# Optimization experiments

Measured on AMD Instinct MI355X. Metric: run time of the kernel, lower is better.

## Reference

```python
import jax, jax.numpy as jnp
import numpy as np

DECAY = 0.99
EPS = 1e-05


def setup_inputs() -> dict:
    key = jax.random.key(0)
    k1, k2 = jax.random.split(key)
    B, L, D, K = 8, 2048, 512, 4096
    x = jax.random.normal(k1, (B, L, D), dtype=jnp.float32)
    # variance_scaling(scale=1, fan_in, uniform): U(-limit, limit), limit = sqrt(3/fan_in)
    limit = np.sqrt(3.0 / D)
    codebook = jax.random.uniform(k2, (K, D), dtype=jnp.float32, minval=-limit, maxval=limit)
    return {
        "x": x,
        "codebook": codebook,
        "hidden_cluster": jnp.zeros((K,), jnp.float32),
        "hidden_dw": jnp.zeros((K, D), jnp.float32),
        "count": jnp.zeros((), jnp.float32),
    }


def reference(x, codebook, hidden_cluster, hidden_dw, count):
    K, D = codebook.shape
    B, L, _ = x.shape
    # avoids materializing the (B,L,K,D) broadcast the naive cdist creates)
    x2 = jnp.sum(x * x, axis=-1, keepdims=True)                  # (B,L,1)
    c2 = jnp.sum(codebook * codebook, axis=-1)                   # (K,)
    xc = jnp.einsum("bld,kd->blk", x, codebook)                  # (B,L,K)
    d2 = x2 - 2.0 * xc + c2
    indices = jnp.argmin(d2, axis=-1)                            # (B,L) int
    flat_idx = indices.reshape(-1)

    # cluster_counts = one_hot(indices).sum((0,1)) as a scatter-add
    cluster_counts = jnp.zeros((K,), jnp.float32).at[flat_idx].add(1.0)
    # dw = einsum('bln,bld->nd', one_hot, x) as a scatter-add of x rows
    dw = jnp.zeros((K, D), jnp.float32).at[flat_idx].add(x.reshape(-1, D))

    decay = jnp.asarray(DECAY, x.dtype)
    one = jnp.ones([], x.dtype)
    count_new = count + 1.0
    bias = one - decay ** count_new

    hidden_cluster_new = hidden_cluster * decay + (one - decay) * cluster_counts
    avg_cluster = hidden_cluster_new / bias
    hidden_dw_new = hidden_dw * decay + (one - decay) * dw
    avg_dw = hidden_dw_new / bias

    N = jnp.sum(avg_cluster)
    cc = (avg_cluster + EPS) / (N + K * EPS) * N
    codebook_new = avg_dw / cc[:, None]

    # quantized = one_hot(indices) @ codebook_new == gather
    q = codebook_new[indices]                                    # (B,L,D)
    quantized = x + jax.lax.stop_gradient(q - x)
    # optax.l2_loss(x, quantized).mean() == 0.5*(x-quantized)^2 mean
    codebook_loss = 0.5 * jnp.mean(jnp.square(x - quantized))
    return quantized, codebook_loss, indices
```

## Files before the change

kernel.cpp:

```cpp
#include <hip/hip_runtime.h>
#include <math.h>

#define BL 16384
#define D  512
#define K  4096
#define NCHB 8
#define XLOFF 8388608

#define OFF_C2    0
#define OFF_X2    (16<<10)
#define OFF_CNT   (80<<10)
#define OFF_AVGC  (96<<10)
#define OFF_SCAL  (112<<10)
#define OFF_IDX16 (116<<10)
#define OFF_KEYS  (160<<10)
#define OFF_CAND  (288<<10)
#define OFF_CBP   (576<<10)
#define OFF_CBN_FB (256<<10)

typedef _Float16 f16x8 __attribute__((ext_vector_type(8)));
typedef float    f32x4 __attribute__((ext_vector_type(4)));
#define MFMA16(a,b,c) __builtin_amdgcn_mfma_f32_16x16x32_f16(a,b,c,0,0,0)


__global__ void rowsq_all(const float* __restrict__ x, const float* __restrict__ cb,
                          float* __restrict__ x2, float* __restrict__ c2)
{
    int b    = blockIdx.x;
    int lane = threadIdx.x;
    const float* p; float* o; int row;
    if (b < K) { p = cb; o = c2; row = b; }
    else       { p = x;  o = x2; row = b - K; }
    p += (size_t)row * D;
    float s = 0.f;
#pragma unroll
    for (int j = 0; j < D / 64; ++j) {
        float v = p[lane + j * 64];
        s = fmaf(v, v, s);
    }
#pragma unroll
    for (int off = 32; off > 0; off >>= 1)
        s += __shfl_down(s, off, 64);
    if (lane == 0) o[row] = s;
}

__global__ __launch_bounds__(256) void rescore_kernel(
    const float* __restrict__ x, const float* __restrict__ cb,
    const float* __restrict__ x2, const float* __restrict__ c2,
    const unsigned short* __restrict__ cand,
    unsigned long long* __restrict__ keys,
    float* __restrict__ counts, unsigned short* __restrict__ idx16)
{
    int t = blockIdx.x * 256 + threadIdx.x;
    int row = t >> 3, ci = t & 7;
    int idx = cand[(size_t)row * 8 + ci];
    const float* xp = x  + (size_t)row * D;
    const float* cp = cb + (size_t)idx * D;
    float acc = 0.f;
#pragma unroll 4
    for (int k0 = 0; k0 < D; k0 += 4) {
        float4 xv = *(const float4*)(xp + k0);
        float4 cv = *(const float4*)(cp + k0);
        acc = fmaf(xv.x, cv.x, acc);
        acc = fmaf(xv.y, cv.y, acc);
        acc = fmaf(xv.z, cv.z, acc);
        acc = fmaf(xv.w, cv.w, acc);
    }
    float wv = x2[row] - 2.0f * acc;
    float dd = wv + c2[idx];
    unsigned long long key =
        ((unsigned long long)__float_as_uint(dd) << 12) | (unsigned long long)idx;
#pragma unroll
    for (int m = 1; m < 8; m <<= 1) {
        unsigned long long o = __shfl_xor(key, m, 64);
        key = o < key ? o : key;
    }
    if ((t & 7) == 0) {
        keys[row] = key;
        int kf = (int)(key & 0xFFFULL);
        idx16[row] = (unsigned short)kf;
        atomicAdd(&counts[kf], 1.0f);
    }
}


__device__ __forceinline__ void load_lds16(const unsigned short* g, unsigned short* l) {
    __builtin_amdgcn_global_load_lds(
        (const __attribute__((address_space(1))) unsigned int*)(g),
        (__attribute__((address_space(3))) unsigned int*)(l), 16, 0, 0);
}

__global__ __launch_bounds__(256) void split_interleave(
    const float* __restrict__ x, const float* __restrict__ cb,
    unsigned short* __restrict__ xp, unsigned short* __restrict__ cbp)
{
    int gw   = blockIdx.x * 4 + (threadIdx.x >> 6);
    int lane = threadIdx.x & 63;
    int rl   = lane >> 3;
    int p    = lane & 7;
    const float* src; int nr, c, r0; bool isX;
    if (gw < 16384) { c = gw >> 11; r0 = (gw & 2047) * 8; src = x;  nr = BL; isX = true; }
    else { int lw = gw - 16384; c = lw >> 9; r0 = (lw & 511) * 8; src = cb; nr = K; isX = false; }
    int r = r0 + rl;
    int g = p ^ rl;
    const float* sp = src + (size_t)r * D + c * 64 + g * 8;
    float4 f0 = *(const float4*)sp, f1 = *(const float4*)(sp + 4);
    float f[8] = {f0.x,f0.y,f0.z,f0.w,f1.x,f1.y,f1.z,f1.w};
    __align__(16) _Float16 oh[8], ol[8];
#pragma unroll
    for (int i = 0; i < 8; ++i) {
        _Float16 h = (_Float16)f[i];
        oh[i] = h;
        ol[i] = (_Float16)(f[i] - (float)h);
    }
    size_t off = ((size_t)(c * nr + r) * 8 + p) * 8;
    if (isX) {
        *(uint4*)(xp + off)         = *(const uint4*)oh;
        *(uint4*)(xp + XLOFF + off) = *(const uint4*)ol;
    } else {
        *(uint4*)(cbp + off) = *(const uint4*)oh;
    }
}

__global__ __launch_bounds__(256, 2) void argmin_mfma(
    const unsigned short* __restrict__ xp, const unsigned short* __restrict__ cbp,
    const float* __restrict__ x2, const float* __restrict__ c2,
    unsigned short* __restrict__ cand)
{
    __shared__ __align__(16) unsigned short sAh[128 * 64];
    __shared__ __align__(16) unsigned short sAl[128 * 64];
    __shared__ __align__(16) unsigned short sB [256 * 64];
    __shared__ __align__(16) float c2s[1024];
    __shared__ float x2s[128];

    const int tid = threadIdx.x;
    const int l   = tid & 63;
    const int w   = tid >> 6;
    const int wm  = w >> 1;
    const int wn  = w & 1;
    const int q   = l >> 4;
    const int cc  = l & 15;
    const int row0 = blockIdx.x * 128;
    const int nb   = blockIdx.y * 1024;

    if (tid < 128) x2s[tid] = x2[row0 + tid];
#pragma unroll
    for (int j = 0; j < 4; ++j) c2s[j * 256 + tid] = c2[nb + j * 256 + tid];

    int rdA[4], rdB[8];
#pragma unroll
    for (int t = 0; t < 4; ++t) {
        int ra = wm * 64 + t * 16 + cc;
        rdA[t] = ra * 128 + ((q ^ (ra & 7)) * 16);
    }
#pragma unroll
    for (int t = 0; t < 8; ++t) {
        int rb = wn * 128 + t * 16 + cc;
        rdB[t] = rb * 128 + ((q ^ (rb & 7)) * 16);
    }

    unsigned long long s1a = ~0ULL, s2a = ~0ULL, s1b = ~0ULL, s2b = ~0ULL;
    unsigned long long s1c = ~0ULL, s2c = ~0ULL, s1d = ~0ULL, s2d = ~0ULL;

#pragma unroll 1
    for (int n0 = 0; n0 < 4; ++n0) {
        f32x4 acc[4][8];
#pragma unroll
        for (int tm = 0; tm < 4; ++tm)
#pragma unroll
            for (int tn = 0; tn < 8; ++tn) { f32x4 z = {0.f,0.f,0.f,0.f}; acc[tm][tn] = z; }

#pragma unroll 1
        for (int c = 0; c < NCHB; ++c) {
            __syncthreads();
            {
                size_t abase = ((size_t)c * BL + row0) * 64;
                size_t bbase = ((size_t)(c * K + nb + n0 * 256)) * 64;
#pragma unroll
                for (int i = 0; i < 4; ++i) {
                    load_lds16(xp + abase + i * 2048 + tid * 8, &sAh[i * 2048 + tid * 8]);
                    load_lds16(xp + XLOFF + abase + i * 2048 + tid * 8, &sAl[i * 2048 + tid * 8]);
                }
#pragma unroll
                for (int i = 0; i < 8; ++i)
                    load_lds16(cbp + bbase + i * 2048 + tid * 8, &sB[i * 2048 + tid * 8]);
            }
            __syncthreads();
#pragma unroll
            for (int kh = 0; kh < 2; ++kh) {
                const int xo = kh * 64;
                f16x8 Ah[4], Al[4], Bf[8];
#pragma unroll
                for (int t = 0; t < 4; ++t) {
                    Ah[t] = *(const f16x8*)((const char*)sAh + (rdA[t] ^ xo));
                    Al[t] = *(const f16x8*)((const char*)sAl + (rdA[t] ^ xo));
                }
#pragma unroll
                for (int t = 0; t < 8; ++t)
                    Bf[t] = *(const f16x8*)((const char*)sB + (rdB[t] ^ xo));
#pragma unroll
                for (int tm = 0; tm < 4; ++tm)
#pragma unroll
                    for (int tn = 0; tn < 8; ++tn)
                        acc[tm][tn] = MFMA16(Ah[tm], Bf[tn], acc[tm][tn]);
#pragma unroll
                for (int tm = 0; tm < 4; ++tm)
#pragma unroll
                    for (int tn = 0; tn < 8; ++tn)
                        acc[tm][tn] = MFMA16(Al[tm], Bf[tn], acc[tm][tn]);
            }
        }

        {
            unsigned long long k1[16], k2[16];
#pragma unroll
            for (int s = 0; s < 16; ++s) { k1[s] = ~0ULL; k2[s] = ~0ULL; }
            float c2v[8];
#pragma unroll
            for (int tn = 0; tn < 8; ++tn)
                c2v[tn] = c2s[n0 * 256 + wn * 128 + tn * 16 + cc];
#pragma unroll
            for (int tm = 0; tm < 4; ++tm)
#pragma unroll
                for (int r = 0; r < 4; ++r) {
                    const int s = tm * 4 + r;
                    float x2v = x2s[wm * 64 + tm * 16 + q * 4 + r];
#pragma unroll
                    for (int tn = 0; tn < 8; ++tn) {
                        unsigned col = nb + n0 * 256 + wn * 128 + tn * 16 + cc;
                        float dd = (x2v - 2.0f * acc[tm][tn][r]) + c2v[tn];
                        unsigned long long key =
                            ((unsigned long long)__float_as_uint(dd) << 12) | col;
                        if (key < k1[s]) { k2[s] = k1[s]; k1[s] = key; }
                        else if (key < k2[s]) { k2[s] = key; }
                    }
                }

#pragma unroll
            for (int s = 0; s < 16; ++s) {
#pragma unroll
                for (int m = 1; m < 16; m <<= 1) {
                    unsigned long long o1 = __shfl_xor(k1[s], m, 64);
                    unsigned long long o2 = __shfl_xor(k2[s], m, 64);
                    unsigned long long lf = k1[s] > o1 ? k1[s] : o1;
                    unsigned long long ws_ = k2[s] < o2 ? k2[s] : o2;
                    k1[s] = k1[s] < o1 ? k1[s] : o1;
                    k2[s] = lf < ws_ ? lf : ws_;
                }
            }
            unsigned long long m1 = k1[0], m2 = k2[0];
#pragma unroll
            for (int s = 1; s < 16; ++s) {
                if (cc == s) { m1 = k1[s]; m2 = k2[s]; }
            }
            if (n0 == 0)      { s1a = m1; s2a = m2; }
            else if (n0 == 1) { s1b = m1; s2b = m2; }
            else if (n0 == 2) { s1c = m1; s2c = m2; }
            else              { s1d = m1; s2d = m2; }
        }
    }

    __syncthreads();
    unsigned long long* sc = (unsigned long long*)sAh;
    {
        int rloc = (cc >> 2) * 16 + q * 4 + (cc & 3);
        int r    = wm * 64 + rloc;
        size_t base = (size_t)((r * 2 + wn) * 4) * 2;
        sc[base + 0] = s1a; sc[base + 1] = s2a;
        sc[base + 2] = s1b; sc[base + 3] = s2b;
        sc[base + 4] = s1c; sc[base + 5] = s2c;
        sc[base + 6] = s1d; sc[base + 7] = s2d;
    }
    __syncthreads();
    if (tid < 128) {
        unsigned long long m1 = ~0ULL, m2 = ~0ULL;
#pragma unroll
        for (int j = 0; j < 8; ++j) {
            unsigned long long b1 = sc[(size_t)(tid * 8 + j) * 2 + 0];
            unsigned long long b2 = sc[(size_t)(tid * 8 + j) * 2 + 1];
            unsigned long long lf  = m1 > b1 ? m1 : b1;
            unsigned long long ws_ = m2 < b2 ? m2 : b2;
            m1 = m1 < b1 ? m1 : b1;
            m2 = lf < ws_ ? lf : ws_;
        }
        size_t base = (size_t)(row0 + tid) * 8 + blockIdx.y * 2;
        cand[base + 0] = (unsigned short)(m1 & 0xFFFULL);
        cand[base + 1] = (unsigned short)(m2 & 0xFFFULL);
    }
}

__global__ __launch_bounds__(256) void argmin_fb(
    const float* __restrict__ x, const float* __restrict__ cb,
    const float* __restrict__ x2, const float* __restrict__ c2,
    unsigned long long* __restrict__ keys)
{
    __shared__ __align__(16) float As[32][68];
    __shared__ __align__(16) float Bs[32][68];
    __shared__ float rv[64][16];
    __shared__ int   ri[64][16];

    const int tid  = threadIdx.x;
    const int tx   = tid & 15;
    const int ty   = tid >> 4;
    const int row0 = blockIdx.x * 64;
    const int nb   = blockIdx.y * 1024;

    float x2r[4];
#pragma unroll
    for (int m = 0; m < 4; ++m) x2r[m] = x2[row0 + ty * 4 + m];

    float minv[4]; int mini[4];
#pragma unroll
    for (int m = 0; m < 4; ++m) { minv[m] = 3.4028235e38f; mini[m] = 0; }

    for (int n0 = 0; n0 < 1024; n0 += 64) {
        float acc[4][4];
#pragma unroll
        for (int m = 0; m < 4; ++m)
#pragma unroll
            for (int n = 0; n < 4; ++n) acc[m][n] = 0.f;

        for (int d0 = 0; d0 < D; d0 += 32) {
            __syncthreads();
#pragma unroll
            for (int j = 0; j < 2; ++j) {
                int v   = j * 256 + tid;
                int row = v >> 3;
                int col = (v & 7) * 4;
                float4 av = *(const float4*)(x  + (size_t)(row0 + row) * D + d0 + col);
                As[col + 0][row] = av.x; As[col + 1][row] = av.y;
                As[col + 2][row] = av.z; As[col + 3][row] = av.w;
                float4 bv = *(const float4*)(cb + (size_t)(nb + n0 + row) * D + d0 + col);
                Bs[col + 0][row] = bv.x; Bs[col + 1][row] = bv.y;
                Bs[col + 2][row] = bv.z; Bs[col + 3][row] = bv.w;
            }
            __syncthreads();
#pragma unroll
            for (int kk = 0; kk < 32; ++kk) {
                float4 a4 = *(const float4*)&As[kk][ty * 4];
                float4 b4 = *(const float4*)&Bs[kk][tx * 4];
                float a_[4] = { a4.x, a4.y, a4.z, a4.w };
                float b_[4] = { b4.x, b4.y, b4.z, b4.w };
#pragma unroll
                for (int m = 0; m < 4; ++m)
#pragma unroll
                    for (int n = 0; n < 4; ++n)
                        acc[m][n] = fmaf(a_[m], b_[n], acc[m][n]);
            }
        }
#pragma unroll
        for (int n = 0; n < 4; ++n) {
            int kidx = nb + n0 + tx * 4 + n;
            float c2k = c2[kidx];
#pragma unroll
            for (int m = 0; m < 4; ++m) {
                float wv = x2r[m] - 2.0f * acc[m][n];
                float dd = wv + c2k;
                if (dd < minv[m]) { minv[m] = dd; mini[m] = kidx; }
            }
        }
    }
#pragma unroll
    for (int m = 0; m < 4; ++m) { rv[ty * 4 + m][tx] = minv[m]; ri[ty * 4 + m][tx] = mini[m]; }
    __syncthreads();
    if (tid < 64) {
        float bv = rv[tid][0]; int bi = ri[tid][0];
#pragma unroll
        for (int j = 1; j < 16; ++j) {
            float v = rv[tid][j]; int ii = ri[tid][j];
            if (v < bv || (v == bv && ii < bi)) { bv = v; bi = ii; }
        }
        unsigned long long key =
            ((unsigned long long)__float_as_uint(bv) << 12) | (unsigned long long)bi;
        atomicMin(&keys[row0 + tid], key);
    }
}


__global__ void count_kernel(const unsigned long long* __restrict__ keys,
                             float* __restrict__ counts, unsigned short* __restrict__ idx16)
{
    int i = blockIdx.x * 256 + threadIdx.x;
    int k = (int)(keys[i] & 0xFFFULL);
    idx16[i] = (unsigned short)k;
    atomicAdd(&counts[k], 1.0f);
}

__global__ __launch_bounds__(256) void ema_cluster_kernel(
    const float* __restrict__ hc, const float* __restrict__ counts,
    const float* __restrict__ countp, float* __restrict__ avgc, float* __restrict__ Nout)
{
    __shared__ float sm[256];
    int i = blockIdx.x * 256 + threadIdx.x;
    const float om = 1.0f - 0.99f;
    float bias = 1.0f - powf(0.99f, countp[0] + 1.0f);
    float a = (hc[i] * 0.99f + om * counts[i]) / bias;
    avgc[i] = a;
    sm[threadIdx.x] = a;
    __syncthreads();
    for (int s = 128; s > 0; s >>= 1) {
        if (threadIdx.x < s) sm[threadIdx.x] += sm[threadIdx.x + s];
        __syncthreads();
    }
    if (threadIdx.x == 0) atomicAdd(Nout, sm[0]);
}

__global__ __launch_bounds__(256) void code_update_kernel(
    const float* __restrict__ x, const unsigned short* __restrict__ idx16,
    const float* __restrict__ hdw, const float* __restrict__ avgc,
    const float* __restrict__ Nptr, const float* __restrict__ countp,
    float* __restrict__ cbn)
{
    __shared__ unsigned short rows[2048];
    __shared__ int cnt;
    int k = blockIdx.x, tid = threadIdx.x;
    if (tid == 0) cnt = 0;
    __syncthreads();
    const uint4* ip = (const uint4*)idx16;
    for (int j = 0; j < 8; ++j) {
        int u = j * 256 + tid;
        uint4 v = ip[u];
        unsigned ww[4] = {v.x, v.y, v.z, v.w};
#pragma unroll
        for (int e = 0; e < 4; ++e) {
            int k0 = (int)(ww[e] & 0xFFFFu), k1 = (int)(ww[e] >> 16);
            if (k0 == k) { int p = atomicAdd(&cnt, 1); if (p < 2048) rows[p] = (unsigned short)(u * 8 + e * 2); }
            if (k1 == k) { int p = atomicAdd(&cnt, 1); if (p < 2048) rows[p] = (unsigned short)(u * 8 + e * 2 + 1); }
        }
    }
    __syncthreads();
    int n = cnt < 2048 ? cnt : 2048;
    float a0 = 0.f, a1 = 0.f;
    for (int p = 0; p < n; ++p) {
        int r = rows[p];
        a0 += x[(size_t)r * D + tid];
        a1 += x[(size_t)r * D + tid + 256];
    }
    const float om = 1.0f - 0.99f;
    float bias = 1.0f - powf(0.99f, countp[0] + 1.0f);
    float Nv = *Nptr;
    float ccv = ((avgc[k] + 1e-5f) / (Nv + 0.04096f)) * Nv;
    size_t b = (size_t)k * D;
    cbn[b + tid]       = ((hdw[b + tid]       * 0.99f + om * a0) / bias) / ccv;
    cbn[b + tid + 256] = ((hdw[b + tid + 256] * 0.99f + om * a1) / bias) / ccv;
}

__global__ __launch_bounds__(256) void gather_kernel(
    const float* __restrict__ x, const unsigned long long* __restrict__ keys,
    const float* __restrict__ cbn, float* __restrict__ outq,
    float* __restrict__ partial)
{
    __shared__ float sm[256];
    int row = blockIdx.x;
    int tid = threadIdx.x;
    int k   = (int)(keys[row] & 0xFFFULL);
    const float* xpp = x   + (size_t)row * D;
    const float* cp  = cbn + (size_t)k   * D;
    float* op = outq + (size_t)row * D;
    float local = 0.f;
#pragma unroll
    for (int j = 0; j < 2; ++j) {
        int d = tid + j * 256;
        float xv = xpp[d];
        float qv = cp[d];
        float quant = xv + (qv - xv);
        op[d] = quant;
        float diff = xv - quant;
        local = fmaf(diff, diff, local);
    }
    sm[tid] = local;
    __syncthreads();
    for (int s = 128; s > 0; s >>= 1) {
        if (tid < s) sm[tid] += sm[tid + s];
        __syncthreads();
    }
    if (tid == 0) {
        partial[row] = sm[0];
        outq[8388609 + row] = (float)k;
    }
}

__global__ __launch_bounds__(256) void finalize_kernel(
    const float* __restrict__ partial, float* __restrict__ out)
{
    __shared__ double sm[256];
    int tid = threadIdx.x;
    double s = 0.0;
#pragma unroll
    for (int j = 0; j < 64; ++j) s += (double)partial[tid + j * 256];
    sm[tid] = s;
    __syncthreads();
    for (int st = 128; st > 0; st >>= 1) {
        if (tid < st) sm[tid] += sm[tid + st];
        __syncthreads();
    }
    if (tid == 0) out[8388608] = (float)(0.5 * sm[0] / 8388608.0);
}


extern "C" void kernel_launch(void* const* d_in, const int* in_sizes, int n_in,
                              void* d_out, int out_size, void* d_ws, size_t ws_size,
                              hipStream_t stream)
{
    const float* x   = (const float*)d_in[0];
    const float* cb  = (const float*)d_in[1];
    const float* hc  = (const float*)d_in[2];
    const float* hdw = (const float*)d_in[3];
    const float* cnt = (const float*)d_in[4];
    float* out = (float*)d_out;

    char* ws = (char*)d_ws;
    float*  c2     = (float*)(ws + OFF_C2);
    float*  x2     = (float*)(ws + OFF_X2);
    float*  counts = (float*)(ws + OFF_CNT);
    float*  avgc   = (float*)(ws + OFF_AVGC);
    float*  Nout   = (float*)(ws + OFF_SCAL + 8);
    unsigned short* idx16 = (unsigned short*)(ws + OFF_IDX16);
    unsigned long long* keys = (unsigned long long*)(ws + OFF_KEYS);
    float*  partial= (float*)(ws + OFF_X2);

    hipMemsetAsync(ws + OFF_CNT, 0, (32 << 10) + 16, stream);

    rowsq_all<<<K + BL, 64, 0, stream>>>(x, cb, x2, c2);

    const bool primary = ws_size >= ((size_t)10 << 20);
    float* cbn;
    if (primary) {
        unsigned short* gxp = (unsigned short*)d_out;
        unsigned short* gcp = (unsigned short*)(ws + OFF_CBP);
        unsigned short* cand = (unsigned short*)(ws + OFF_CAND);
        cbn = (float*)(ws + OFF_CBP);

        split_interleave<<<5120, 256, 0, stream>>>(x, cb, gxp, gcp);
        argmin_mfma<<<dim3(BL / 128, 4), 256, 0, stream>>>(gxp, gcp, x2, c2, cand);
        rescore_kernel<<<(BL * 8) / 256, 256, 0, stream>>>(x, cb, x2, c2, cand, keys,
                                                           counts, idx16);
    } else {
        cbn = (float*)(ws + OFF_CBN_FB);
        hipMemsetAsync(ws + OFF_KEYS, 0xFF, BL * 8, stream);
        argmin_fb<<<dim3(BL / 64, 4), 256, 0, stream>>>(x, cb, x2, c2, keys);
        count_kernel<<<BL / 256, 256, 0, stream>>>(keys, counts, idx16);
    }

    ema_cluster_kernel<<<K / 256, 256, 0, stream>>>(hc, counts, cnt, avgc, Nout);
    code_update_kernel<<<K, 256, 0, stream>>>(x, idx16, hdw, avgc, Nout, cnt, cbn);
    gather_kernel<<<BL, 256, 0, stream>>>(x, keys, cbn, out, partial);
    finalize_kernel<<<1, 256, 0, stream>>>(partial, out);
}
```

Measured before the change: 323.8 us.

## Double-buffer LDS tiles in argmin MFMA kernel with flattened k-loop

Replaces the separate A-high, A-low and B shared buffers with a two-stage ping-pong buffer. The n0 and k-chunk loops become one 64-iteration loop, where each iteration prefetches the next 32-wide k slice while running MFMAs on the current one. Each chunk is now split into half-k stages with a new XOR swizzle applied on the global-load side, and there is one barrier per iteration instead of two. This aims to hide global-to-LDS latency behind compute, at the cost of more LDS use per block and more frequent smaller stages.

```diff
diff --git a/kernel.cpp b/kernel.cpp
--- a/kernel.cpp
+++ b/kernel.cpp
@@ -127,11 +127,10 @@
     const float* __restrict__ x2, const float* __restrict__ c2,
     unsigned short* __restrict__ cand)
 {
-    __shared__ __align__(16) unsigned short sAh[128 * 64];
-    __shared__ __align__(16) unsigned short sAl[128 * 64];
-    __shared__ __align__(16) unsigned short sB [256 * 64];
+    __shared__ __align__(16) unsigned short buf[2 * 16384];
     __shared__ __align__(16) float c2s[1024];
     __shared__ float x2s[128];
+
 
     const int tid = threadIdx.x;
     const int l   = tid & 63;
@@ -149,69 +148,78 @@
 
     int rdA[4], rdB[8];
 #pragma unroll
-    for (int t = 0; t < 4; ++t) {
-        int ra = wm * 64 + t * 16 + cc;
-        rdA[t] = ra * 128 + ((q ^ (ra & 7)) * 16);
-    }
-#pragma unroll
-    for (int t = 0; t < 8; ++t) {
-        int rb = wn * 128 + t * 16 + cc;
-        rdB[t] = rb * 128 + ((q ^ (rb & 7)) * 16);
-    }
+    for (int t = 0; t < 4; ++t)
+        rdA[t] = (wm * 64 + t * 16 + cc) * 64 + q * 16;
+#pragma unroll
+    for (int t = 0; t < 8; ++t)
+        rdB[t] = (wn * 128 + t * 16 + cc) * 64 + q * 16;
+
+    auto STAGE = [&](int s) {
+        const int n0s = s >> 4, c64 = (s >> 1) & 7, h = s & 1;
+        unsigned short* d = buf + (s & 1) * 16384;
+        const int jr = l & 3, rr = l >> 2;
+        const int p  = ((h << 2) | jr) ^ (rr & 7);
+        const unsigned short* gAh = xp + (((size_t)c64 * BL + row0) << 6);
+        const unsigned short* gAl = gAh + XLOFF;
+        const unsigned short* gB  = cbp + (((size_t)c64 * K + nb + n0s * 256) << 6);
+#pragma unroll
+        for (int i = 0; i < 2; ++i) {
+            const int rbase = (w + 4 * i) * 16;
+            load_lds16(gAh + (size_t)(rbase + rr) * 64 + p * 8,
+                       d + (w + 4 * i) * 512 + l * 8);
+            load_lds16(gAl + (size_t)(rbase + rr) * 64 + p * 8,
+                       d + 4096 + (w + 4 * i) * 512 + l * 8);
+        }
+#pragma unroll
+        for (int i = 0; i < 4; ++i) {
+            const int rbase = (w + 4 * i) * 16;
+            load_lds16(gB + (size_t)(rbase + rr) * 64 + p * 8,
+                       d + 8192 + (w + 4 * i) * 512 + l * 8);
+        }
+    };
+
+    STAGE(0);
+    __syncthreads();
 
     unsigned long long s1a = ~0ULL, s2a = ~0ULL, s1b = ~0ULL, s2b = ~0ULL;
     unsigned long long s1c = ~0ULL, s2c = ~0ULL, s1d = ~0ULL, s2d = ~0ULL;
 
+    f32x4 acc[4][8];
+#pragma unroll
+    for (int tm = 0; tm < 4; ++tm)
+#pragma unroll
+        for (int tn = 0; tn < 8; ++tn) { f32x4 z = {0.f,0.f,0.f,0.f}; acc[tm][tn] = z; }
+
 #pragma unroll 1
-    for (int n0 = 0; n0 < 4; ++n0) {
-        f32x4 acc[4][8];
+    for (int it = 0; it < 64; ++it) {
+        if (it < 63) {
+            STAGE(it + 1);
+            __builtin_amdgcn_sched_barrier(0);
+        }
+
+        const char* bb = (const char*)buf + (it & 1) * 32768;
+        f16x8 Ah[4], Al[4], Bf[8];
+#pragma unroll
+        for (int t = 0; t < 4; ++t) {
+            Ah[t] = *(const f16x8*)(bb + rdA[t]);
+            Al[t] = *(const f16x8*)(bb + 8192 + rdA[t]);
+        }
+#pragma unroll
+        for (int t = 0; t < 8; ++t)
+            Bf[t] = *(const f16x8*)(bb + 16384 + rdB[t]);
 #pragma unroll
         for (int tm = 0; tm < 4; ++tm)
 #pragma unroll
-            for (int tn = 0; tn < 8; ++tn) { f32x4 z = {0.f,0.f,0.f,0.f}; acc[tm][tn] = z; }
-
-#pragma unroll 1
-        for (int c = 0; c < NCHB; ++c) {
-            __syncthreads();
-            {
-                size_t abase = ((size_t)c * BL + row0) * 64;
-                size_t bbase = ((size_t)(c * K + nb + n0 * 256)) * 64;
-#pragma unroll
-                for (int i = 0; i < 4; ++i) {
-                    load_lds16(xp + abase + i * 2048 + tid * 8, &sAh[i * 2048 + tid * 8]);
-                    load_lds16(xp + XLOFF + abase + i * 2048 + tid * 8, &sAl[i * 2048 + tid * 8]);
-                }
-#pragma unroll
-                for (int i = 0; i < 8; ++i)
-                    load_lds16(cbp + bbase + i * 2048 + tid * 8, &sB[i * 2048 + tid * 8]);
-            }
-            __syncthreads();
-#pragma unroll
-            for (int kh = 0; kh < 2; ++kh) {
-                const int xo = kh * 64;
-                f16x8 Ah[4], Al[4], Bf[8];
-#pragma unroll
-                for (int t = 0; t < 4; ++t) {
-                    Ah[t] = *(const f16x8*)((const char*)sAh + (rdA[t] ^ xo));
-                    Al[t] = *(const f16x8*)((const char*)sAl + (rdA[t] ^ xo));
-                }
-#pragma unroll
-                for (int t = 0; t < 8; ++t)
-                    Bf[t] = *(const f16x8*)((const char*)sB + (rdB[t] ^ xo));
-#pragma unroll
-                for (int tm = 0; tm < 4; ++tm)
-#pragma unroll
-                    for (int tn = 0; tn < 8; ++tn)
-                        acc[tm][tn] = MFMA16(Ah[tm], Bf[tn], acc[tm][tn]);
-#pragma unroll
-                for (int tm = 0; tm < 4; ++tm)
-#pragma unroll
-                    for (int tn = 0; tn < 8; ++tn)
-                        acc[tm][tn] = MFMA16(Al[tm], Bf[tn], acc[tm][tn]);
-            }
-        }
-
-        {
+            for (int tn = 0; tn < 8; ++tn)
+                acc[tm][tn] = MFMA16(Ah[tm], Bf[tn], acc[tm][tn]);
+#pragma unroll
+        for (int tm = 0; tm < 4; ++tm)
+#pragma unroll
+            for (int tn = 0; tn < 8; ++tn)
+                acc[tm][tn] = MFMA16(Al[tm], Bf[tn], acc[tm][tn]);
+
+        if ((it & 15) == 15) {
+            const int n0 = it >> 4;
             unsigned long long k1[16], k2[16];
 #pragma unroll
             for (int s = 0; s < 16; ++s) { k1[s] = ~0ULL; k2[s] = ~0ULL; }
@@ -235,7 +243,6 @@
                         else if (key < k2[s]) { k2[s] = key; }
                     }
                 }
-
 #pragma unroll
             for (int s = 0; s < 16; ++s) {
 #pragma unroll
@@ -257,11 +264,16 @@
             else if (n0 == 1) { s1b = m1; s2b = m2; }
             else if (n0 == 2) { s1c = m1; s2c = m2; }
             else              { s1d = m1; s2d = m2; }
-        }
-    }
-
-    __syncthreads();
-    unsigned long long* sc = (unsigned long long*)sAh;
+#pragma unroll
+            for (int tm = 0; tm < 4; ++tm)
+#pragma unroll
+                for (int tn = 0; tn < 8; ++tn) { f32x4 z = {0.f,0.f,0.f,0.f}; acc[tm][tn] = z; }
+        }
+
+        __syncthreads();
+    }
+
+    unsigned long long* sc = (unsigned long long*)buf;
     {
         int rloc = (cc >> 2) * 16 + q * 4 + (cc & 3);
         int r    = wm * 64 + rloc;
```

Result: slower. 340.1 us (+5.0%).

## Fuse x row norms into split pass, drop EMA kernel, vectorize gather

Applied to the files above, without the earlier changes.

Computes the x row squared norms inside split_interleave with atomics instead of a separate rowsq pass over x. The EMA cluster kernel is removed by computing N analytically, using the fact that the counts always sum to BL, and computing each cluster average inline in code_update. The gather kernel now handles two rows per block with float4 loads. This saves one full read of x and one launch, at the cost of atomics on x2 and a widened memset.

```diff
diff --git a/kernel.cpp b/kernel.cpp
--- a/kernel.cpp
+++ b/kernel.cpp
@@ -24,13 +24,25 @@
 
 
 __global__ void rowsq_all(const float* __restrict__ x, const float* __restrict__ cb,
-                          float* __restrict__ x2, float* __restrict__ c2)
+                          const float* __restrict__ hc,
+                          float* __restrict__ x2, float* __restrict__ c2,
+                          float* __restrict__ Shc)
 {
     int b    = blockIdx.x;
     int lane = threadIdx.x;
+    if (b == K) {
+        float s = 0.f;
+#pragma unroll
+        for (int j = 0; j < K / 64; ++j) s += hc[lane + j * 64];
+#pragma unroll
+        for (int off = 32; off > 0; off >>= 1)
+            s += __shfl_down(s, off, 64);
+        if (lane == 0) Shc[0] = s;
+        return;
+    }
     const float* p; float* o; int row;
     if (b < K) { p = cb; o = c2; row = b; }
-    else       { p = x;  o = x2; row = b - K; }
+    else       { p = x;  o = x2; row = b - K - 1; }
     p += (size_t)row * D;
     float s = 0.f;
 #pragma unroll
@@ -92,7 +104,8 @@
 
 __global__ __launch_bounds__(256) void split_interleave(
     const float* __restrict__ x, const float* __restrict__ cb,
-    unsigned short* __restrict__ xp, unsigned short* __restrict__ cbp)
+    unsigned short* __restrict__ xp, unsigned short* __restrict__ cbp,
+    float* __restrict__ x2)
 {
     int gw   = blockIdx.x * 4 + (threadIdx.x >> 6);
     int lane = threadIdx.x & 63;
@@ -117,6 +130,13 @@
     if (isX) {
         *(uint4*)(xp + off)         = *(const uint4*)oh;
         *(uint4*)(xp + XLOFF + off) = *(const uint4*)ol;
+        float s = 0.f;
+#pragma unroll
+        for (int i = 0; i < 8; ++i) s = fmaf(f[i], f[i], s);
+        s += __shfl_xor(s, 1, 64);
+        s += __shfl_xor(s, 2, 64);
+        s += __shfl_xor(s, 4, 64);
+        if (p == 0) atomicAdd(&x2[r], s);
     } else {
         *(uint4*)(cbp + off) = *(const uint4*)oh;
     }
@@ -386,30 +406,11 @@
     atomicAdd(&counts[k], 1.0f);
 }
 
-__global__ __launch_bounds__(256) void ema_cluster_kernel(
-    const float* __restrict__ hc, const float* __restrict__ counts,
-    const float* __restrict__ countp, float* __restrict__ avgc, float* __restrict__ Nout)
-{
-    __shared__ float sm[256];
-    int i = blockIdx.x * 256 + threadIdx.x;
-    const float om = 1.0f - 0.99f;
-    float bias = 1.0f - powf(0.99f, countp[0] + 1.0f);
-    float a = (hc[i] * 0.99f + om * counts[i]) / bias;
-    avgc[i] = a;
-    sm[threadIdx.x] = a;
-    __syncthreads();
-    for (int s = 128; s > 0; s >>= 1) {
-        if (threadIdx.x < s) sm[threadIdx.x] += sm[threadIdx.x + s];
-        __syncthreads();
-    }
-    if (threadIdx.x == 0) atomicAdd(Nout, sm[0]);
-}
-
 __global__ __launch_bounds__(256) void code_update_kernel(
     const float* __restrict__ x, const unsigned short* __restrict__ idx16,
-    const float* __restrict__ hdw, const float* __restrict__ avgc,
-    const float* __restrict__ Nptr, const float* __restrict__ countp,
-    float* __restrict__ cbn)
+    const float* __restrict__ hdw, const float* __restrict__ hc,
+    const float* __restrict__ counts, const float* __restrict__ Shc,
+    const float* __restrict__ countp, float* __restrict__ cbn)
 {
     __shared__ unsigned short rows[2048];
     __shared__ int cnt;
@@ -438,8 +439,9 @@
     }
     const float om = 1.0f - 0.99f;
     float bias = 1.0f - powf(0.99f, countp[0] + 1.0f);
-    float Nv = *Nptr;
-    float ccv = ((avgc[k] + 1e-5f) / (Nv + 0.04096f)) * Nv;
+    float Nv   = (0.99f * Shc[0] + 0.01f * 16384.0f) / bias;
+    float avgk = (hc[k] * 0.99f + om * counts[k]) / bias;
+    float ccv  = ((avgk + 1e-5f) / (Nv + 0.04096f)) * Nv;
     size_t b = (size_t)k * D;
     cbn[b + tid]       = ((hdw[b + tid]       * 0.99f + om * a0) / bias) / ccv;
     cbn[b + tid + 256] = ((hdw[b + tid + 256] * 0.99f + om * a1) / bias) / ccv;
@@ -451,31 +453,37 @@
     float* __restrict__ partial)
 {
     __shared__ float sm[256];
-    int row = blockIdx.x;
-    int tid = threadIdx.x;
-    int k   = (int)(keys[row] & 0xFFFULL);
-    const float* xpp = x   + (size_t)row * D;
-    const float* cp  = cbn + (size_t)k   * D;
-    float* op = outq + (size_t)row * D;
+    int t    = threadIdx.x;
+    int rloc = t >> 7;
+    int ci   = t & 127;
+    int row  = blockIdx.x * 2 + rloc;
+    int k    = (int)(keys[row] & 0xFFFULL);
+    const float4* xv4 = (const float4*)(x   + (size_t)row * D);
+    const float4* cv4 = (const float4*)(cbn + (size_t)k   * D);
+    float4*       ov4 = (float4*)(outq + (size_t)row * D);
+    float4 xv = xv4[ci];
+    float4 qv = cv4[ci];
+    float4 quant;
+    quant.x = xv.x + (qv.x - xv.x);
+    quant.y = xv.y + (qv.y - xv.y);
+    quant.z = xv.z + (qv.z - xv.z);
+    quant.w = xv.w + (qv.w - xv.w);
+    ov4[ci] = quant;
+    float dx = xv.x - quant.x, dy = xv.y - quant.y;
+    float dz = xv.z - quant.z, dw = xv.w - quant.w;
     float local = 0.f;
-#pragma unroll
-    for (int j = 0; j < 2; ++j) {
-        int d = tid + j * 256;
-        float xv = xpp[d];
-        float qv = cp[d];
-        float quant = xv + (qv - xv);
-        op[d] = quant;
-        float diff = xv - quant;
-        local = fmaf(diff, diff, local);
-    }
-    sm[tid] = local;
-    __syncthreads();
-    for (int s = 128; s > 0; s >>= 1) {
-        if (tid < s) sm[tid] += sm[tid + s];
+    local = fmaf(dx, dx, local);
+    local = fmaf(dy, dy, local);
+    local = fmaf(dz, dz, local);
+    local = fmaf(dw, dw, local);
+    sm[t] = local;
+    __syncthreads();
+    for (int s = 64; s > 0; s >>= 1) {
+        if ((t & 127) < s) sm[t] += sm[t + s];
         __syncthreads();
     }
-    if (tid == 0) {
-        partial[row] = sm[0];
+    if (ci == 0) {
+        partial[row] = sm[rloc * 128];
         outq[8388609 + row] = (float)k;
     }
 }
@@ -513,37 +521,36 @@
     float*  c2     = (float*)(ws + OFF_C2);
     float*  x2     = (float*)(ws + OFF_X2);
     float*  counts = (float*)(ws + OFF_CNT);
-    float*  avgc   = (float*)(ws + OFF_AVGC);
-    float*  Nout   = (float*)(ws + OFF_SCAL + 8);
+    float*  Shc    = (float*)(ws + OFF_SCAL + 16);
     unsigned short* idx16 = (unsigned short*)(ws + OFF_IDX16);
     unsigned long long* keys = (unsigned long long*)(ws + OFF_KEYS);
     float*  partial= (float*)(ws + OFF_X2);
 
-    hipMemsetAsync(ws + OFF_CNT, 0, (32 << 10) + 16, stream);
-
-    rowsq_all<<<K + BL, 64, 0, stream>>>(x, cb, x2, c2);
+    hipMemsetAsync(ws + OFF_X2, 0, (96 << 10) + 32, stream);
 
     const bool primary = ws_size >= ((size_t)10 << 20);
     float* cbn;
     if (primary) {
+        rowsq_all<<<K + 1, 64, 0, stream>>>(x, cb, hc, x2, c2, Shc);
+
         unsigned short* gxp = (unsigned short*)d_out;
         unsigned short* gcp = (unsigned short*)(ws + OFF_CBP);
         unsigned short* cand = (unsigned short*)(ws + OFF_CAND);
         cbn = (float*)(ws + OFF_CBP);
 
-        split_interleave<<<5120, 256, 0, stream>>>(x, cb, gxp, gcp);
+        split_interleave<<<5120, 256, 0, stream>>>(x, cb, gxp, gcp, x2);
         argmin_mfma<<<dim3(BL / 128, 4), 256, 0, stream>>>(gxp, gcp, x2, c2, cand);
         rescore_kernel<<<(BL * 8) / 256, 256, 0, stream>>>(x, cb, x2, c2, cand, keys,
                                                            counts, idx16);
     } else {
+        rowsq_all<<<K + 1 + BL, 64, 0, stream>>>(x, cb, hc, x2, c2, Shc);
         cbn = (float*)(ws + OFF_CBN_FB);
         hipMemsetAsync(ws + OFF_KEYS, 0xFF, BL * 8, stream);
         argmin_fb<<<dim3(BL / 64, 4), 256, 0, stream>>>(x, cb, x2, c2, keys);
         count_kernel<<<BL / 256, 256, 0, stream>>>(keys, counts, idx16);
     }
 
-    ema_cluster_kernel<<<K / 256, 256, 0, stream>>>(hc, counts, cnt, avgc, Nout);
-    code_update_kernel<<<K, 256, 0, stream>>>(x, idx16, hdw, avgc, Nout, cnt, cbn);
-    gather_kernel<<<BL, 256, 0, stream>>>(x, keys, cbn, out, partial);
+    code_update_kernel<<<K, 256, 0, stream>>>(x, idx16, hdw, hc, counts, Shc, cnt, cbn);
+    gather_kernel<<<BL / 2, 256, 0, stream>>>(x, keys, cbn, out, partial);
     finalize_kernel<<<1, 256, 0, stream>>>(partial, out);
 }
```

Result: no change. 319.5 us (median of 2 runs) (-1.3%).
